# Kernel optimization log

Hardware: AMD Instinct MI355X
Metric: run time of the kernel (lower is better)

Reference implementation:

```python
import jax, jax.numpy as jnp
import numpy as np
from jax import lax

# db4 decomposition low-pass filter (pywt convention, ascending index)
DEC_LO = np.array([-0.010597401784997278, 0.032883011666982945, 0.030841381835986965,
                   -0.18703481171888114, -0.02798376941698385, 0.6308807679295904,
                   0.7148465705525415, 0.23037781330885523], dtype=np.float32)
L = 8
REC_LO = DEC_LO[::-1].copy()
DEC_HI = (REC_LO * ((-1.0) ** (np.arange(L) + 1))).astype(np.float32)
REC_HI = DEC_HI[::-1].copy()


def _dwt_last(x, lo, hi):
    """Single-level DWT along last axis, pywt 'symmetric' mode.
    Returns (cA, cD), each (..., (N+L-1)//2)."""
    ext = jnp.pad(x, [(0, 0)] * (x.ndim - 1) + [(L - 1, L - 1)], mode='symmetric')[..., 1:]
    z = ext.reshape(-1, 1, ext.shape[-1])
    # correlation with flipped filter == true convolution
    k = jnp.stack([lo[::-1], hi[::-1]])[:, None, :]  # (2,1,L)
    y = lax.conv_general_dilated(z, k, (2,), 'VALID', dimension_numbers=('NCH', 'OIH', 'NCH'))
    y = y.reshape(x.shape[:-1] + (2, y.shape[-1]))
    return y[..., 0, :], y[..., 1, :]


def _idwt_last(cA, cD, lo, hi):
    """Single-level inverse DWT along last axis (pywt upsampling convolution)."""
    n = cA.shape[-1]
    up = jnp.zeros(cA.shape[:-1] + (2, 2 * n - 1), cA.dtype)
    up = up.at[..., 0, ::2].set(cA).at[..., 1, ::2].set(cD)
    z = up.reshape(-1, 2, 2 * n - 1)
    k = jnp.stack([lo[::-1], hi[::-1]])[None, :, :]  # (1,2,L) -> sum of lo/hi branches
    y = lax.conv_general_dilated(z, k, (1,), [(L - 1, L - 1)], dimension_numbers=('NCH', 'OIH', 'NCH'))
    y = y[:, 0, L - 2: 2 * n]  # length 2n - L + 2
    return y.reshape(cA.shape[:-1] + (2 * n - L + 2,))


def dwt2d(x):
    lo, hi = jnp.asarray(DEC_LO), jnp.asarray(DEC_HI)
    a, d = _dwt_last(x, lo, hi)                       # along W
    aa, da = _dwt_last(a.swapaxes(-1, -2), lo, hi)    # along H
    ad, dd = _dwt_last(d.swapaxes(-1, -2), lo, hi)
    LL = aa.swapaxes(-1, -2)
    LH = da.swapaxes(-1, -2)   # cH: detail along H, approx along W
    HL = ad.swapaxes(-1, -2)   # cV: approx along H, detail along W
    HH = dd.swapaxes(-1, -2)
    return LL, LH, HL, HH


def idwt2d(LL, LH, HL, HH):
    lo, hi = jnp.asarray(REC_LO), jnp.asarray(REC_HI)
    a = _idwt_last(LL.swapaxes(-1, -2), LH.swapaxes(-1, -2), lo, hi).swapaxes(-1, -2)  # along H
    d = _idwt_last(HL.swapaxes(-1, -2), HH.swapaxes(-1, -2), lo, hi).swapaxes(-1, -2)
    return _idwt_last(a, d, lo, hi)  # along W


def attention_weight(x, c1w, c1b, c2w, gamma, beta, rmean, rvar):
    """x: (b, w, c, h). Max/mean pool over dim 1, 1x1 conv 2->1, depthwise conv1d
    over c channels, BatchNorm1d (eval), sigmoid gate."""
    feat = jnp.stack([x.max(axis=1), x.mean(axis=1)], axis=1)  # (b,2,c,h)
    y = jnp.einsum('i,bich->bch', c1w.reshape(2), feat) + c1b[0]  # (b,c,h)
    C = y.shape[1]
    p = (c2w.shape[-1] - 1) // 2
    y = lax.conv_general_dilated(y, c2w, (1,), [(p, p)], feature_group_count=C,
                                 dimension_numbers=('NCH', 'OIH', 'NCH'))
    y = (y - rmean[:, None]) * lax.rsqrt(rvar[:, None] + 1e-5) * gamma[:, None] + beta[:, None]
    return x * jax.nn.sigmoid(y)[:, None]


def _forward(x, lh_c1w, lh_c1b, lh_c2w, lh_g, lh_b, lh_m, lh_v,
             hl_c1w, hl_c1b, hl_c2w, hl_g, hl_b, hl_m, hl_v):
    LL, LH, HL, HH = dwt2d(x)
    LHp = attention_weight(LH.transpose(0, 3, 1, 2), lh_c1w, lh_c1b, lh_c2w, lh_g, lh_b, lh_m, lh_v).transpose(0, 2, 3, 1)
    HLp = attention_weight(HL.transpose(0, 2, 1, 3), hl_c1w, hl_c1b, hl_c2w, hl_g, hl_b, hl_m, hl_v).transpose(0, 2, 1, 3)
    rec = idwt2d(LL, LHp, HLp, HH)
    H, W = x.shape[-2], x.shape[-1]
    return x + rec[..., :H, :W]


def setup_inputs() -> dict:
    key = jax.random.key(0)
    ks = jax.random.split(key, 16)
    B, C, H, W, K = 8, 64, 512, 512, 3
    d = {"x": jax.random.normal(ks[0], (B, C, H, W), dtype=jnp.float32)}
    for i, pre in enumerate(["lh", "hl"]):
        base = 1 + 7 * i
        d[pre + "_c1w"] = jax.random.normal(ks[base + 0], (1, 2, 1, 1), dtype=jnp.float32) * 0.5
        d[pre + "_c1b"] = jax.random.normal(ks[base + 1], (1,), dtype=jnp.float32) * 0.1
        d[pre + "_c2w"] = jax.random.normal(ks[base + 2], (C, 1, K), dtype=jnp.float32) * 0.3
        d[pre + "_g"] = jnp.ones((C,), dtype=jnp.float32)
        d[pre + "_b"] = jnp.zeros((C,), dtype=jnp.float32)
        d[pre + "_m"] = jax.random.normal(ks[base + 3], (C,), dtype=jnp.float32) * 0.1
        d[pre + "_v"] = jax.random.uniform(ks[base + 4], (C,), dtype=jnp.float32, minval=0.5, maxval=1.5)
    return d


def reference(x, lh_c1w, lh_c1b, lh_c2w, lh_g, lh_b, lh_m, lh_v,
              hl_c1w, hl_c1b, hl_c2w, hl_g, hl_b, hl_m, hl_v):
    return _forward(x, lh_c1w, lh_c1b, lh_c2w, lh_g, lh_b, lh_m, lh_v,
                    hl_c1w, hl_c1b, hl_c2w, hl_g, hl_b, hl_m, hl_v)
```

## Files before the change

### kernel.cpp

```cpp
#include <hip/hip_runtime.h>

typedef _Float16 h16;
typedef _Float16 h16x2 __attribute__((ext_vector_type(2)));
typedef _Float16 h16x4 __attribute__((ext_vector_type(4)));
typedef _Float16 h16x8 __attribute__((ext_vector_type(8)));
typedef float f32x4 __attribute__((ext_vector_type(4)));

#if __has_builtin(__builtin_amdgcn_fdot2)
#define FDOT2(a, b, c) __builtin_amdgcn_fdot2((a), (b), (c), false)
#else
static __device__ __forceinline__ float FDOT2(h16x2 a, h16x2 b, float c) {
  return c + (float)a[0] * (float)b[0] + (float)a[1] * (float)b[1];
}
#endif

#define N_IMG 512
#define C_CH  64
#define H_IN  512
#define W_IN  512
#define NC    259
#define PITP  528
#define S2    ((size_t)NC * PITP)
#define GPIT  264
#define FSTRIP 17
#define LROWS  38

constexpr float DLO[8] = {
  -0.010597401784997278f,  0.032883011666982945f,  0.030841381835986965f, -0.18703481171888114f,
  -0.02798376941698385f,   0.6308807679295904f,    0.7148465705525415f,    0.23037781330885523f};
constexpr float DHI[8] = {
  -0.23037781330885523f,   0.7148465705525415f,   -0.6308807679295904f,   -0.02798376941698385f,
   0.18703481171888114f,   0.030841381835986965f, -0.032883011666982945f, -0.010597401784997278f};
constexpr float RLO[8] = {
   0.23037781330885523f,   0.7148465705525415f,    0.6308807679295904f,   -0.02798376941698385f,
  -0.18703481171888114f,   0.030841381835986965f,  0.032883011666982945f, -0.010597401784997278f};
constexpr float RHI[8] = {
  -0.010597401784997278f, -0.032883011666982945f,  0.030841381835986965f,  0.18703481171888114f,
  -0.02798376941698385f,  -0.6308807679295904f,    0.7148465705525415f,   -0.23037781330885523f};

__global__ __launch_bounds__(512) void k_fwd(const float* __restrict__ x,
                                             h16* __restrict__ wsh,
                                             float* __restrict__ stat) {
  __shared__ h16 sad[LROWS * PITP];
  const int p = blockIdx.x;
  const int w = (p & 7) * 1088 + (p >> 3);
  const int bc = w / FSTRIP;
  const int bx = w - bc * FSTRIP;
  const int h0 = bx * 16;
  const int hcount = min(16, NC - h0);
  const int nrows = 2 * hcount + 6;
  const int tid = threadIdx.x;
  const int wave = tid >> 6, lane = tid & 63;
  const float* xim = x + (size_t)bc * (H_IN * (size_t)W_IN);

  for (int j = wave; j < nrows; j += 8) {
    int r = 2 * h0 - 6 + j;
    r = r < 0 ? -r - 1 : (r >= H_IN ? 2 * H_IN - 1 - r : r);
    const float* xrow = xim + (size_t)r * W_IN;
    h16* sj = sad + j * PITP;
    const int base = lane ? 8 * lane - 8 : 0;
    const float4 q0 = *(const float4*)(xrow + base);
    const float4 q1 = *(const float4*)(xrow + base + 4);
    const float4 q2 = *(const float4*)(xrow + base + 8);
    const float4 q3 = *(const float4*)(xrow + base + 12);
    const float v[16] = {q0.x, q0.y, q0.z, q0.w, q1.x, q1.y, q1.z, q1.w,
                         q2.x, q2.y, q2.z, q2.w, q3.x, q3.y, q3.z, q3.w};
    if (lane == 0) {
      h16x8 o;
#pragma unroll
      for (int i = 0; i < 4; ++i) {
        float a = 0.f, d = 0.f;
#pragma unroll
        for (int m = 0; m < 8; ++m) {
          int pp = 2 * i + 1 - m; pp = pp < 0 ? -pp - 1 : pp;
          const float t = v[pp];
          a += DLO[m] * t; d += DHI[m] * t;
        }
        o[2 * i] = (h16)a; o[2 * i + 1] = (h16)d;
      }
      *(h16x8*)(sj) = o;
    } else {
      h16x8 o;
#pragma unroll
      for (int k = 0; k < 4; ++k) {
        float a = 0.f, d = 0.f;
#pragma unroll
        for (int m = 0; m < 8; ++m) {
          const float t = v[2 * k + 9 - m];
          a += DLO[m] * t; d += DHI[m] * t;
        }
        o[2 * k] = (h16)a; o[2 * k + 1] = (h16)d;
      }
      *(h16x8*)(sj + 8 * lane) = o;
      if (lane == 63) {
#pragma unroll
        for (int i = 256; i < 259; ++i) {
          float a = 0.f, d = 0.f;
#pragma unroll
          for (int m = 0; m < 8; ++m) {
            int pp = 2 * i + 1 - m; pp = pp >= 512 ? 1023 - pp : pp;
            const float t = v[pp - 496];
            a += DLO[m] * t; d += DHI[m] * t;
          }
          h16x2 o2; o2[0] = (h16)a; o2[1] = (h16)d;
          *(h16x2*)(sj + 2 * i) = o2;
        }
      }
    }
  }
  __syncthreads();

  const size_t obase = (size_t)bc * S2;
  const int ntask = hcount * 66;
  float rlh[3][4], rhl[3][4];
#pragma unroll
  for (int slot = 0; slot < 3; ++slot) {
    const int task = tid + slot * 512;
    if (task < ntask) {
      const int dh = task / 66, pq = task - dh * 66;
      h16x2 a0 = {0, 0}, a1 = {0, 0}, a2_ = {0, 0}, a3 = {0, 0};
#pragma unroll
      for (int m = 0; m < 8; ++m) {
        const int j = 2 * dh + 7 - m;
        const h16x8 pr = *(const h16x8*)(sad + j * PITP + 8 * pq);
        const h16x2 cf = {(h16)DHI[m], (h16)DLO[m]};
        const h16x2 p0 = {pr[0], pr[1]}, p1 = {pr[2], pr[3]};
        const h16x2 p2 = {pr[4], pr[5]}, p3 = {pr[6], pr[7]};
        a0 += cf * p0; a1 += cf * p1; a2_ += cf * p2; a3 += cf * p3;
      }
      if (pq == 64) { a3 = (h16x2){0, 0}; }
      if (pq == 65) { a0 = a1 = a2_ = a3 = (h16x2){0, 0}; }
      h16x8 o = {a0[0], a0[1], a1[0], a1[1], a2_[0], a2_[1], a3[0], a3[1]};
      *(h16x8*)(wsh + obase + (size_t)(h0 + dh) * PITP + 8 * pq) = o;
      rlh[slot][0] = (float)a0[0]; rlh[slot][1] = (float)a1[0];
      rlh[slot][2] = (float)a2_[0]; rlh[slot][3] = (float)a3[0];
      rhl[slot][0] = (float)a0[1]; rhl[slot][1] = (float)a1[1];
      rhl[slot][2] = (float)a2_[1]; rhl[slot][3] = (float)a3[1];
    }
  }
  __syncthreads();

  float* scol = (float*)sad;
  float* prmx = scol + 16 * 264;
  float* prsm = prmx + 1056;
#pragma unroll
  for (int slot = 0; slot < 3; ++slot) {
    const int task = tid + slot * 512;
    if (task < ntask) {
      const int dh = task / 66, pq = task - dh * 66;
      if (pq < 66) {
        *(float4*)(scol + dh * 264 + 4 * pq) =
            {rhl[slot][0], rhl[slot][1], rhl[slot][2], rhl[slot][3]};
      }
      if (pq == 65) {
        prmx[task] = -3.4e38f; prsm[task] = 0.f;
      } else {
        const float m01 = fmaxf(rlh[slot][0], rlh[slot][1]);
        const float m23 = (pq == 64) ? rlh[slot][2] : fmaxf(rlh[slot][2], rlh[slot][3]);
        prmx[task] = fmaxf(m01, m23);
        prsm[task] = rlh[slot][0] + rlh[slot][1] + rlh[slot][2] + rlh[slot][3];
      }
    }
  }
  __syncthreads();
  float* rsM = stat;
  float* rsS = stat + (size_t)N_IMG * 264;
  float* cpM = rsS + (size_t)N_IMG * 264;
  float* cpS = cpM + (size_t)N_IMG * FSTRIP * 264;
  for (int hh = wave; hh < hcount; hh += 8) {
    float m = prmx[hh * 66 + lane], s = prsm[hh * 66 + lane];
    if (lane == 0) {
      m = fmaxf(m, fmaxf(prmx[hh * 66 + 64], prmx[hh * 66 + 65]));
      s += prsm[hh * 66 + 64] + prsm[hh * 66 + 65];
    }
#pragma unroll
    for (int off = 32; off; off >>= 1) {
      m = fmaxf(m, __shfl_xor(m, off)); s += __shfl_xor(s, off);
    }
    if (lane == 0) {
      rsM[bc * 264 + h0 + hh] = m;
      rsS[bc * 264 + h0 + hh] = s;
    }
  }
  if (tid < 264) {
    float m = -3.4e38f, s = 0.f;
    for (int dh = 0; dh < hcount; ++dh) {
      const float vv = scol[dh * 264 + tid]; m = fmaxf(m, vv); s += vv;
    }
    const size_t cb = ((size_t)bc * FSTRIP + bx) * 264 + tid;
    cpM[cb] = m; cpS[cb] = s;
  }
}

__global__ __launch_bounds__(256) void k_gate(
    const float* __restrict__ stat, float* __restrict__ gout,
    const float* lc1w, const float* lc1b, const float* lc2w,
    const float* lg, const float* lb, const float* lm, const float* lv,
    const float* hc1w, const float* hc1b, const float* hc2w,
    const float* hg, const float* hb, const float* hm, const float* hv) {
  __shared__ float cmx[264], csm[264], y0a[264], y0b[264];
  const int bc = blockIdx.x;
  const int tid = threadIdx.x;
  const float* rsM = stat;
  const float* rsS = stat + (size_t)N_IMG * 264;
  const float* cpM = rsS + (size_t)N_IMG * 264;
  const float* cpS = cpM + (size_t)N_IMG * FSTRIP * 264;

  for (int col = tid; col < 264; col += 256) {
    float m = -3.4e38f, s = 0.f;
    for (int st = 0; st < FSTRIP; ++st) {
      const size_t cb = ((size_t)bc * FSTRIP + st) * 264 + col;
      m = fmaxf(m, cpM[cb]); s += cpS[cb];
    }
    cmx[col] = m; csm[col] = s;
  }
  __syncthreads();
  const float lw0 = lc1w[0], lw1 = lc1w[1], lbb0 = lc1b[0];
  const float hw0 = hc1w[0], hw1 = hc1w[1], hbb0 = hc1b[0];
  for (int idx = tid; idx < NC; idx += 256) {
    y0a[idx] = lw0 * rsM[bc * 264 + idx] + lw1 * (rsS[bc * 264 + idx] * (1.f / NC)) + lbb0;
    y0b[idx] = hw0 * cmx[idx] + hw1 * (csm[idx] * (1.f / NC)) + hbb0;
  }
  __syncthreads();
  const int c = bc & (C_CH - 1);
  const float lk0 = lc2w[c * 3], lk1 = lc2w[c * 3 + 1], lk2 = lc2w[c * 3 + 2];
  const float hk0 = hc2w[c * 3], hk1 = hc2w[c * 3 + 1], hk2 = hc2w[c * 3 + 2];
  const float lsc = rsqrtf(lv[c] + 1e-5f) * lg[c], lmu = lm[c], lbe = lb[c];
  const float hsc = rsqrtf(hv[c] + 1e-5f) * hg[c], hmu = hm[c], hbe = hb[c];
  for (int idx = tid; idx < NC; idx += 256) {
    float a = idx > 0 ? y0a[idx - 1] : 0.f;
    float b = y0a[idx];
    float d = idx < NC - 1 ? y0a[idx + 1] : 0.f;
    float y = lk0 * a + lk1 * b + lk2 * d;
    y = (y - lmu) * lsc + lbe;
    gout[(size_t)bc * GPIT + idx] = 1.f / (1.f + expf(-y)) - 1.f;

    a = idx > 0 ? y0b[idx - 1] : 0.f;
    b = y0b[idx];
    d = idx < NC - 1 ? y0b[idx + 1] : 0.f;
    y = hk0 * a + hk1 * b + hk2 * d;
    y = (y - hmu) * hsc + hbe;
    gout[(size_t)N_IMG * GPIT + (size_t)bc * GPIT + idx] = 1.f / (1.f + expf(-y)) - 1.f;
  }
}

__global__ __launch_bounds__(512) void k_inv(const h16* __restrict__ wsh,
                                             const float* __restrict__ gbuf,
                                             const float* __restrict__ x,
                                             float* __restrict__ out) {
  __shared__ h16 sBC[11 * PITP];
  __shared__ h16 ad2[16 * PITP];
  __shared__ h16 sghl16[264];
  const int p = blockIdx.x;
  const int w = (p & 7) * 2048 + (p >> 3);
  const int bc = w >> 5;
  const int t0 = (w & 31) * 16;
  const int u0 = t0 >> 1;
  const int tid = threadIdx.x;
  const h16* sub = wsh + (size_t)bc * S2;
  const float* glh = gbuf + (size_t)bc * GPIT;
  const float* ghl = gbuf + (size_t)N_IMG * GPIT + (size_t)bc * GPIT;

  if (tid < 264) sghl16[tid] = (h16)ghl[tid];

  for (int t = tid; t < 11 * 66; t += 512) {
    const int j = t / 66, pq = t - j * 66;
    const int u = u0 + j;
    const h16 glH = (h16)glh[u];
    const h16x2 cf = {glH, (h16)1.0f};
    const h16x8 pr = *(const h16x8*)(sub + (size_t)u * PITP + 8 * pq);
    h16x2 r0 = cf * (h16x2){pr[0], pr[1]};
    h16x2 r1 = cf * (h16x2){pr[2], pr[3]};
    h16x2 r2 = cf * (h16x2){pr[4], pr[5]};
    h16x2 r3 = cf * (h16x2){pr[6], pr[7]};
    h16x8 o = {r0[0], r0[1], r1[0], r1[1], r2[0], r2[1], r3[0], r3[1]};
    *(h16x8*)(sBC + j * PITP + 8 * pq) = o;
  }
  __syncthreads();

  for (int task = tid; task < 16 * 132; task += 512) {
    const int dt = task / 132, pq = task - dt * 132;
    const int par = dt & 1, lj0 = dt >> 1;
    h16x2 acc0 = {0, 0}, acc1 = {0, 0};
#pragma unroll
    for (int jj = 0; jj < 4; ++jj) {
      const int lj = lj0 + 3 - jj;
      const h16x2 cf = {(h16)(par ? RHI[1 + 2 * jj] : RHI[2 * jj]),
                        (h16)(par ? RLO[1 + 2 * jj] : RLO[2 * jj])};
      const h16x4 pr = *(const h16x4*)(sBC + lj * PITP + 4 * pq);
      acc0 += cf * (h16x2){pr[0], pr[1]};
      acc1 += cf * (h16x2){pr[2], pr[3]};
    }
    const h16x2 g2 = *(const h16x2*)(sghl16 + 2 * pq);
    const h16x2 cg0 = {(h16)1.0f, g2[0]};
    const h16x2 cg1 = {(h16)1.0f, g2[1]};
    acc0 *= cg0; acc1 *= cg1;
    h16x4 o = {acc0[0], acc0[1], acc1[0], acc1[1]};
    *(h16x4*)(ad2 + dt * PITP + 4 * pq) = o;
  }
  __syncthreads();

  for (int task = tid; task < 16 * 128; task += 512) {
    const int dt = task >> 7, r = task & 127;
    const h16* row = ad2 + dt * PITP + 4 * r;
    const h16x4 w0 = *(const h16x4*)(row);
    const h16x4 w1 = *(const h16x4*)(row + 4);
    const h16x2 w2 = *(const h16x2*)(row + 8);
    const h16x2 P[5] = {{w0[0], w0[1]}, {w0[2], w0[3]},
                        {w1[0], w1[1]}, {w1[2], w1[3]}, w2};
    float vv[4];
#pragma unroll
    for (int k = 0; k < 4; ++k) {
      const int base = k >> 1, par = k & 1;
      float s = 0.f;
#pragma unroll
      for (int jj = 0; jj < 4; ++jj) {
        const h16x2 cf = {(h16)RLO[par + 2 * jj], (h16)RHI[par + 2 * jj]};
        s = FDOT2(P[base + 3 - jj], cf, s);
      }
      vv[k] = s;
    }
    const size_t orow = ((size_t)bc * H_IN + (size_t)(t0 + dt)) * W_IN + 4 * r;
    const f32x4 xv = __builtin_nontemporal_load((const f32x4*)(x + orow));
    f32x4 ov;
    ov.x = 2.f * xv.x + vv[0]; ov.y = 2.f * xv.y + vv[1];
    ov.z = 2.f * xv.z + vv[2]; ov.w = 2.f * xv.w + vv[3];
    __builtin_nontemporal_store(ov, (f32x4*)(out + orow));
  }
}

extern "C" void kernel_launch(void* const* d_in, const int* in_sizes, int n_in,
                              void* d_out, int out_size, void* d_ws, size_t ws_size,
                              hipStream_t stream) {
  const float* x = (const float*)d_in[0];
  h16* wsh = (h16*)d_ws;
  float* statf = (float*)(wsh + (size_t)N_IMG * S2);
  float* gbuf = statf + 2 * (size_t)N_IMG * 264 + 2 * (size_t)N_IMG * FSTRIP * 264;
  float* out = (float*)d_out;

  k_fwd<<<dim3(FSTRIP * N_IMG), 512, 0, stream>>>(x, wsh, statf);
  k_gate<<<dim3(N_IMG), 256, 0, stream>>>(
      statf, gbuf,
      (const float*)d_in[1], (const float*)d_in[2], (const float*)d_in[3],
      (const float*)d_in[4], (const float*)d_in[5], (const float*)d_in[6], (const float*)d_in[7],
      (const float*)d_in[8], (const float*)d_in[9], (const float*)d_in[10],
      (const float*)d_in[11], (const float*)d_in[12], (const float*)d_in[13], (const float*)d_in[14]);
  k_inv<<<dim3(32 * N_IMG), 512, 0, stream>>>(wsh, gbuf, x, out);
}
```

Baseline: 370.3 us.

## Stream forward DWT over half-images with a ring buffer; enlarge inverse tiles

```diff
diff --git a/kernel.cpp b/kernel.cpp
--- a/kernel.cpp
+++ b/kernel.cpp
@@ -22,8 +22,7 @@
 #define PITP  528
 #define S2    ((size_t)NC * PITP)
 #define GPIT  264
-#define FSTRIP 17
-#define LROWS  38
+#define RING  38
 
 constexpr float DLO[8] = {
   -0.010597401784997278f,  0.032883011666982945f,  0.030841381835986965f, -0.18703481171888114f,
@@ -41,153 +40,171 @@
 __global__ __launch_bounds__(512) void k_fwd(const float* __restrict__ x,
                                              h16* __restrict__ wsh,
                                              float* __restrict__ stat) {
-  __shared__ h16 sad[LROWS * PITP];
+  __shared__ h16 sad[RING * PITP];
   const int p = blockIdx.x;
-  const int w = (p & 7) * 1088 + (p >> 3);
-  const int bc = w / FSTRIP;
-  const int bx = w - bc * FSTRIP;
-  const int h0 = bx * 16;
-  const int hcount = min(16, NC - h0);
-  const int nrows = 2 * hcount + 6;
+  const int w = (p & 7) * 128 + (p >> 3);
+  const int bc = w >> 1;
+  const int half = w & 1;
+  const int h_begin = half ? 130 : 0;
+  const int h_end = half ? 259 : 130;
   const int tid = threadIdx.x;
   const int wave = tid >> 6, lane = tid & 63;
   const float* xim = x + (size_t)bc * (H_IN * (size_t)W_IN);
-
-  for (int j = wave; j < nrows; j += 8) {
-    int r = 2 * h0 - 6 + j;
-    r = r < 0 ? -r - 1 : (r >= H_IN ? 2 * H_IN - 1 - r : r);
-    const float* xrow = xim + (size_t)r * W_IN;
-    h16* sj = sad + j * PITP;
-    const int base = lane ? 8 * lane - 8 : 0;
-    const float4 q0 = *(const float4*)(xrow + base);
-    const float4 q1 = *(const float4*)(xrow + base + 4);
-    const float4 q2 = *(const float4*)(xrow + base + 8);
-    const float4 q3 = *(const float4*)(xrow + base + 12);
-    const float v[16] = {q0.x, q0.y, q0.z, q0.w, q1.x, q1.y, q1.z, q1.w,
-                         q2.x, q2.y, q2.z, q2.w, q3.x, q3.y, q3.z, q3.w};
-    if (lane == 0) {
-      h16x8 o;
-#pragma unroll
-      for (int i = 0; i < 4; ++i) {
-        float a = 0.f, d = 0.f;
-#pragma unroll
-        for (int m = 0; m < 8; ++m) {
-          int pp = 2 * i + 1 - m; pp = pp < 0 ? -pp - 1 : pp;
-          const float t = v[pp];
-          a += DLO[m] * t; d += DHI[m] * t;
-        }
-        o[2 * i] = (h16)a; o[2 * i + 1] = (h16)d;
-      }
-      *(h16x8*)(sj) = o;
-    } else {
-      h16x8 o;
-#pragma unroll
-      for (int k = 0; k < 4; ++k) {
-        float a = 0.f, d = 0.f;
-#pragma unroll
-        for (int m = 0; m < 8; ++m) {
-          const float t = v[2 * k + 9 - m];
-          a += DLO[m] * t; d += DHI[m] * t;
-        }
-        o[2 * k] = (h16)a; o[2 * k + 1] = (h16)d;
-      }
-      *(h16x8*)(sj + 8 * lane) = o;
-      if (lane == 63) {
-#pragma unroll
-        for (int i = 256; i < 259; ++i) {
-          float a = 0.f, d = 0.f;
-#pragma unroll
-          for (int m = 0; m < 8; ++m) {
-            int pp = 2 * i + 1 - m; pp = pp >= 512 ? 1023 - pp : pp;
-            const float t = v[pp - 496];
-            a += DLO[m] * t; d += DHI[m] * t;
-          }
-          h16x2 o2; o2[0] = (h16)a; o2[1] = (h16)d;
-          *(h16x2*)(sj + 2 * i) = o2;
-        }
-      }
-    }
-  }
-  __syncthreads();
-
   const size_t obase = (size_t)bc * S2;
-  const int ntask = hcount * 66;
-  float rlh[3][4], rhl[3][4];
-#pragma unroll
-  for (int slot = 0; slot < 3; ++slot) {
-    const int task = tid + slot * 512;
-    if (task < ntask) {
-      const int dh = task / 66, pq = task - dh * 66;
-      h16x2 a0 = {0, 0}, a1 = {0, 0}, a2_ = {0, 0}, a3 = {0, 0};
-#pragma unroll
-      for (int m = 0; m < 8; ++m) {
-        const int j = 2 * dh + 7 - m;
-        const h16x8 pr = *(const h16x8*)(sad + j * PITP + 8 * pq);
-        const h16x2 cf = {(h16)DHI[m], (h16)DLO[m]};
-        const h16x2 p0 = {pr[0], pr[1]}, p1 = {pr[2], pr[3]};
-        const h16x2 p2 = {pr[4], pr[5]}, p3 = {pr[6], pr[7]};
-        a0 += cf * p0; a1 += cf * p1; a2_ += cf * p2; a3 += cf * p3;
-      }
-      if (pq == 64) { a3 = (h16x2){0, 0}; }
-      if (pq == 65) { a0 = a1 = a2_ = a3 = (h16x2){0, 0}; }
-      h16x8 o = {a0[0], a0[1], a1[0], a1[1], a2_[0], a2_[1], a3[0], a3[1]};
-      *(h16x8*)(wsh + obase + (size_t)(h0 + dh) * PITP + 8 * pq) = o;
-      rlh[slot][0] = (float)a0[0]; rlh[slot][1] = (float)a1[0];
-      rlh[slot][2] = (float)a2_[0]; rlh[slot][3] = (float)a3[0];
-      rhl[slot][0] = (float)a0[1]; rhl[slot][1] = (float)a1[1];
-      rhl[slot][2] = (float)a2_[1]; rhl[slot][3] = (float)a3[1];
-    }
-  }
-  __syncthreads();
-
-  float* scol = (float*)sad;
-  float* prmx = scol + 16 * 264;
-  float* prsm = prmx + 1056;
-#pragma unroll
-  for (int slot = 0; slot < 3; ++slot) {
-    const int task = tid + slot * 512;
-    if (task < ntask) {
-      const int dh = task / 66, pq = task - dh * 66;
-      if (pq < 66) {
-        *(float4*)(scol + dh * 264 + 4 * pq) =
-            {rhl[slot][0], rhl[slot][1], rhl[slot][2], rhl[slot][3]};
-      }
-      if (pq == 65) {
-        prmx[task] = -3.4e38f; prsm[task] = 0.f;
-      } else {
-        const float m01 = fmaxf(rlh[slot][0], rlh[slot][1]);
-        const float m23 = (pq == 64) ? rlh[slot][2] : fmaxf(rlh[slot][2], rlh[slot][3]);
-        prmx[task] = fmaxf(m01, m23);
-        prsm[task] = rlh[slot][0] + rlh[slot][1] + rlh[slot][2] + rlh[slot][3];
-      }
-    }
-  }
-  __syncthreads();
+
   float* rsM = stat;
   float* rsS = stat + (size_t)N_IMG * 264;
   float* cpM = rsS + (size_t)N_IMG * 264;
-  float* cpS = cpM + (size_t)N_IMG * FSTRIP * 264;
-  for (int hh = wave; hh < hcount; hh += 8) {
-    float m = prmx[hh * 66 + lane], s = prsm[hh * 66 + lane];
-    if (lane == 0) {
-      m = fmaxf(m, fmaxf(prmx[hh * 66 + 64], prmx[hh * 66 + 65]));
-      s += prsm[hh * 66 + 64] + prsm[hh * 66 + 65];
-    }
-#pragma unroll
-    for (int off = 32; off; off >>= 1) {
-      m = fmaxf(m, __shfl_xor(m, off)); s += __shfl_xor(s, off);
-    }
-    if (lane == 0) {
-      rsM[bc * 264 + h0 + hh] = m;
-      rsS[bc * 264 + h0 + hh] = s;
-    }
-  }
+  float* cpS = cpM + (size_t)N_IMG * 2 * 264;
+
+  float c0m[4], c0s[4], c1m[4], c1s[4];
+#pragma unroll
+  for (int k = 0; k < 4; ++k) {
+    c0m[k] = -3.4e38f; c0s[k] = 0.f; c1m[k] = -3.4e38f; c1s[k] = 0.f;
+  }
+
+  int rx_next = 2 * h_begin - 6;
+  for (int h0 = h_begin; h0 < h_end; h0 += 16) {
+    const int hcount = min(16, h_end - h0);
+    const int rx_hi = 2 * (h0 + hcount - 1) + 1;
+
+    for (int j = rx_next + wave; j <= rx_hi; j += 8) {
+      int r = j;
+      r = r < 0 ? -r - 1 : (r >= H_IN ? 2 * H_IN - 1 - r : r);
+      const float* xrow = xim + (size_t)r * W_IN;
+      h16* sj = sad + ((j + RING) % RING) * PITP;
+      const int base = lane ? 8 * lane - 8 : 0;
+      const float4 q0 = *(const float4*)(xrow + base);
+      const float4 q1 = *(const float4*)(xrow + base + 4);
+      const float4 q2 = *(const float4*)(xrow + base + 8);
+      const float4 q3 = *(const float4*)(xrow + base + 12);
+      const float v[16] = {q0.x, q0.y, q0.z, q0.w, q1.x, q1.y, q1.z, q1.w,
+                           q2.x, q2.y, q2.z, q2.w, q3.x, q3.y, q3.z, q3.w};
+      if (lane == 0) {
+        h16x8 o;
+#pragma unroll
+        for (int i = 0; i < 4; ++i) {
+          float a = 0.f, d = 0.f;
+#pragma unroll
+          for (int m = 0; m < 8; ++m) {
+            int pp = 2 * i + 1 - m; pp = pp < 0 ? -pp - 1 : pp;
+            const float t = v[pp];
+            a += DLO[m] * t; d += DHI[m] * t;
+          }
+          o[2 * i] = (h16)a; o[2 * i + 1] = (h16)d;
+        }
+        *(h16x8*)(sj) = o;
+      } else {
+        h16x8 o;
+#pragma unroll
+        for (int k = 0; k < 4; ++k) {
+          float a = 0.f, d = 0.f;
+#pragma unroll
+          for (int m = 0; m < 8; ++m) {
+            const float t = v[2 * k + 9 - m];
+            a += DLO[m] * t; d += DHI[m] * t;
+          }
+          o[2 * k] = (h16)a; o[2 * k + 1] = (h16)d;
+        }
+        *(h16x8*)(sj + 8 * lane) = o;
+        if (lane == 63) {
+#pragma unroll
+          for (int i = 256; i < 259; ++i) {
+            float a = 0.f, d = 0.f;
+#pragma unroll
+            for (int m = 0; m < 8; ++m) {
+              int pp = 2 * i + 1 - m; pp = pp >= 512 ? 1023 - pp : pp;
+              const float t = v[pp - 496];
+              a += DLO[m] * t; d += DHI[m] * t;
+            }
+            h16x2 o2; o2[0] = (h16)a; o2[1] = (h16)d;
+            *(h16x2*)(sj + 2 * i) = o2;
+          }
+        }
+      }
+    }
+    rx_next = rx_hi + 1;
+    __syncthreads();
+
+    for (int dh = wave; dh < hcount; dh += 8) {
+      const int h = h0 + dh;
+      const int s0 = (2 * h + 1) % RING;
+      float rowm = -3.4e38f, rowsum = 0.f;
+#pragma unroll
+      for (int pass = 0; pass < 2; ++pass) {
+        const int pq = lane + 64 * pass;
+        if (pq < 66) {
+          h16x2 a0 = {0, 0}, a1 = {0, 0}, a2_ = {0, 0}, a3 = {0, 0};
+#pragma unroll
+          for (int m = 0; m < 8; ++m) {
+            int slot = s0 - m; slot = slot < 0 ? slot + RING : slot;
+            const h16x8 pr = *(const h16x8*)(sad + slot * PITP + 8 * pq);
+            const h16x2 cf = {(h16)DHI[m], (h16)DLO[m]};
+            a0 += cf * (h16x2){pr[0], pr[1]};
+            a1 += cf * (h16x2){pr[2], pr[3]};
+            a2_ += cf * (h16x2){pr[4], pr[5]};
+            a3 += cf * (h16x2){pr[6], pr[7]};
+          }
+          if (pq == 64) { a3 = (h16x2){0, 0}; }
+          if (pq == 65) { a0 = a1 = a2_ = a3 = (h16x2){0, 0}; }
+          h16x8 o = {a0[0], a0[1], a1[0], a1[1], a2_[0], a2_[1], a3[0], a3[1]};
+          *(h16x8*)(wsh + obase + (size_t)h * PITP + 8 * pq) = o;
+          const float l0 = (float)a0[0], l1 = (float)a1[0];
+          const float l2 = (float)a2_[0], l3 = (float)a3[0];
+          const float g0 = (float)a0[1], g1 = (float)a1[1];
+          const float g2 = (float)a2_[1], g3 = (float)a3[1];
+          if (pq < 65) {
+            const float m01 = fmaxf(l0, l1);
+            const float m23 = (pq == 64) ? l2 : fmaxf(l2, l3);
+            rowm = fmaxf(rowm, fmaxf(m01, m23));
+            rowsum += l0 + l1 + l2 + l3;
+          }
+          if (pass == 0) {
+            c0m[0] = fmaxf(c0m[0], g0); c0s[0] += g0;
+            c0m[1] = fmaxf(c0m[1], g1); c0s[1] += g1;
+            c0m[2] = fmaxf(c0m[2], g2); c0s[2] += g2;
+            c0m[3] = fmaxf(c0m[3], g3); c0s[3] += g3;
+          } else {
+            c1m[0] = fmaxf(c1m[0], g0); c1s[0] += g0;
+            c1m[1] = fmaxf(c1m[1], g1); c1s[1] += g1;
+            c1m[2] = fmaxf(c1m[2], g2); c1s[2] += g2;
+            c1m[3] = fmaxf(c1m[3], g3); c1s[3] += g3;
+          }
+        }
+      }
+#pragma unroll
+      for (int off = 32; off; off >>= 1) {
+        rowm = fmaxf(rowm, __shfl_xor(rowm, off));
+        rowsum += __shfl_xor(rowsum, off);
+      }
+      if (lane == 0) {
+        rsM[bc * 264 + h] = rowm;
+        rsS[bc * 264 + h] = rowsum;
+      }
+    }
+    __syncthreads();
+  }
+
+  float* wbuf = (float*)sad;
+  float* wm = wbuf + wave * 528;
+  float* wsv = wm + 264;
+#pragma unroll
+  for (int k = 0; k < 4; ++k) { wm[4 * lane + k] = c0m[k]; wsv[4 * lane + k] = c0s[k]; }
+  if (lane < 2) {
+#pragma unroll
+    for (int k = 0; k < 4; ++k) {
+      wm[256 + 4 * lane + k] = c1m[k]; wsv[256 + 4 * lane + k] = c1s[k];
+    }
+  }
+  __syncthreads();
   if (tid < 264) {
     float m = -3.4e38f, s = 0.f;
-    for (int dh = 0; dh < hcount; ++dh) {
-      const float vv = scol[dh * 264 + tid]; m = fmaxf(m, vv); s += vv;
-    }
-    const size_t cb = ((size_t)bc * FSTRIP + bx) * 264 + tid;
+#pragma unroll
+    for (int w8 = 0; w8 < 8; ++w8) {
+      m = fmaxf(m, wbuf[w8 * 528 + tid]);
+      s += wbuf[w8 * 528 + 264 + tid];
+    }
+    const size_t cb = ((size_t)bc * 2 + half) * 264 + tid;
     cpM[cb] = m; cpS[cb] = s;
   }
 }
@@ -204,15 +221,13 @@
   const float* rsM = stat;
   const float* rsS = stat + (size_t)N_IMG * 264;
   const float* cpM = rsS + (size_t)N_IMG * 264;
-  const float* cpS = cpM + (size_t)N_IMG * FSTRIP * 264;
+  const float* cpS = cpM + (size_t)N_IMG * 2 * 264;
 
   for (int col = tid; col < 264; col += 256) {
-    float m = -3.4e38f, s = 0.f;
-    for (int st = 0; st < FSTRIP; ++st) {
-      const size_t cb = ((size_t)bc * FSTRIP + st) * 264 + col;
-      m = fmaxf(m, cpM[cb]); s += cpS[cb];
-    }
-    cmx[col] = m; csm[col] = s;
+    const size_t cb0 = ((size_t)bc * 2) * 264 + col;
+    const size_t cb1 = ((size_t)bc * 2 + 1) * 264 + col;
+    cmx[col] = fmaxf(cpM[cb0], cpM[cb1]);
+    csm[col] = cpS[cb0] + cpS[cb1];
   }
   __syncthreads();
   const float lw0 = lc1w[0], lw1 = lc1w[1], lbb0 = lc1b[0];
@@ -248,13 +263,13 @@
                                              const float* __restrict__ gbuf,
                                              const float* __restrict__ x,
                                              float* __restrict__ out) {
-  __shared__ h16 sBC[11 * PITP];
+  __shared__ h16 sBC[19 * PITP];
   __shared__ h16 ad2[16 * PITP];
   __shared__ h16 sghl16[264];
   const int p = blockIdx.x;
-  const int w = (p & 7) * 2048 + (p >> 3);
-  const int bc = w >> 5;
-  const int t0 = (w & 31) * 16;
+  const int w = (p & 7) * 1024 + (p >> 3);
+  const int bc = w >> 4;
+  const int t0 = (w & 15) * 32;
   const int u0 = t0 >> 1;
   const int tid = threadIdx.x;
   const h16* sub = wsh + (size_t)bc * S2;
@@ -263,7 +278,7 @@
 
   if (tid < 264) sghl16[tid] = (h16)ghl[tid];
 
-  for (int t = tid; t < 11 * 66; t += 512) {
+  for (int t = tid; t < 19 * 66; t += 512) {
     const int j = t / 66, pq = t - j * 66;
     const int u = u0 + j;
     const h16 glH = (h16)glh[u];
@@ -278,54 +293,60 @@
   }
   __syncthreads();
 
-  for (int task = tid; task < 16 * 132; task += 512) {
-    const int dt = task / 132, pq = task - dt * 132;
-    const int par = dt & 1, lj0 = dt >> 1;
-    h16x2 acc0 = {0, 0}, acc1 = {0, 0};
-#pragma unroll
-    for (int jj = 0; jj < 4; ++jj) {
-      const int lj = lj0 + 3 - jj;
-      const h16x2 cf = {(h16)(par ? RHI[1 + 2 * jj] : RHI[2 * jj]),
-                        (h16)(par ? RLO[1 + 2 * jj] : RLO[2 * jj])};
-      const h16x4 pr = *(const h16x4*)(sBC + lj * PITP + 4 * pq);
-      acc0 += cf * (h16x2){pr[0], pr[1]};
-      acc1 += cf * (h16x2){pr[2], pr[3]};
-    }
-    const h16x2 g2 = *(const h16x2*)(sghl16 + 2 * pq);
-    const h16x2 cg0 = {(h16)1.0f, g2[0]};
-    const h16x2 cg1 = {(h16)1.0f, g2[1]};
-    acc0 *= cg0; acc1 *= cg1;
-    h16x4 o = {acc0[0], acc0[1], acc1[0], acc1[1]};
-    *(h16x4*)(ad2 + dt * PITP + 4 * pq) = o;
-  }
-  __syncthreads();
-
-  for (int task = tid; task < 16 * 128; task += 512) {
-    const int dt = task >> 7, r = task & 127;
-    const h16* row = ad2 + dt * PITP + 4 * r;
-    const h16x4 w0 = *(const h16x4*)(row);
-    const h16x4 w1 = *(const h16x4*)(row + 4);
-    const h16x2 w2 = *(const h16x2*)(row + 8);
-    const h16x2 P[5] = {{w0[0], w0[1]}, {w0[2], w0[3]},
-                        {w1[0], w1[1]}, {w1[2], w1[3]}, w2};
-    float vv[4];
-#pragma unroll
-    for (int k = 0; k < 4; ++k) {
-      const int base = k >> 1, par = k & 1;
-      float s = 0.f;
+#pragma unroll
+  for (int batch = 0; batch < 2; ++batch) {
+    for (int task = tid; task < 16 * 132; task += 512) {
+      const int dtl = task / 132, pq = task - dtl * 132;
+      const int dt = batch * 16 + dtl;
+      const int par = dt & 1, lj0 = dt >> 1;
+      h16x2 acc0 = {0, 0}, acc1 = {0, 0};
 #pragma unroll
       for (int jj = 0; jj < 4; ++jj) {
-        const h16x2 cf = {(h16)RLO[par + 2 * jj], (h16)RHI[par + 2 * jj]};
-        s = FDOT2(P[base + 3 - jj], cf, s);
-      }
-      vv[k] = s;
-    }
-    const size_t orow = ((size_t)bc * H_IN + (size_t)(t0 + dt)) * W_IN + 4 * r;
-    const f32x4 xv = __builtin_nontemporal_load((const f32x4*)(x + orow));
-    f32x4 ov;
-    ov.x = 2.f * xv.x + vv[0]; ov.y = 2.f * xv.y + vv[1];
-    ov.z = 2.f * xv.z + vv[2]; ov.w = 2.f * xv.w + vv[3];
-    __builtin_nontemporal_store(ov, (f32x4*)(out + orow));
+        const int lj = lj0 + 3 - jj;
+        const h16x2 cf = {(h16)(par ? RHI[1 + 2 * jj] : RHI[2 * jj]),
+                          (h16)(par ? RLO[1 + 2 * jj] : RLO[2 * jj])};
+        const h16x4 pr = *(const h16x4*)(sBC + lj * PITP + 4 * pq);
+        acc0 += cf * (h16x2){pr[0], pr[1]};
+        acc1 += cf * (h16x2){pr[2], pr[3]};
+      }
+      const h16x2 g2 = *(const h16x2*)(sghl16 + 2 * pq);
+      const h16x2 cg0 = {(h16)1.0f, g2[0]};
+      const h16x2 cg1 = {(h16)1.0f, g2[1]};
+      acc0 *= cg0; acc1 *= cg1;
+      h16x4 o = {acc0[0], acc0[1], acc1[0], acc1[1]};
+      *(h16x4*)(ad2 + dtl * PITP + 4 * pq) = o;
+    }
+    __syncthreads();
+
+    for (int task = tid; task < 16 * 128; task += 512) {
+      const int dtl = task >> 7, r = task & 127;
+      const h16* row = ad2 + dtl * PITP + 4 * r;
+      const h16x4 w0 = *(const h16x4*)(row);
+      const h16x4 w1 = *(const h16x4*)(row + 4);
+      const h16x2 w2 = *(const h16x2*)(row + 8);
+      const h16x2 P[5] = {{w0[0], w0[1]}, {w0[2], w0[3]},
+                          {w1[0], w1[1]}, {w1[2], w1[3]}, w2};
+      float vv[4];
+#pragma unroll
+      for (int k = 0; k < 4; ++k) {
+        const int base = k >> 1, par = k & 1;
+        float s = 0.f;
+#pragma unroll
+        for (int jj = 0; jj < 4; ++jj) {
+          const h16x2 cf = {(h16)RLO[par + 2 * jj], (h16)RHI[par + 2 * jj]};
+          s = FDOT2(P[base + 3 - jj], cf, s);
+        }
+        vv[k] = s;
+      }
+      const size_t orow =
+          ((size_t)bc * H_IN + (size_t)(t0 + batch * 16 + dtl)) * W_IN + 4 * r;
+      const f32x4 xv = __builtin_nontemporal_load((const f32x4*)(x + orow));
+      f32x4 ov;
+      ov.x = 2.f * xv.x + vv[0]; ov.y = 2.f * xv.y + vv[1];
+      ov.z = 2.f * xv.z + vv[2]; ov.w = 2.f * xv.w + vv[3];
+      __builtin_nontemporal_store(ov, (f32x4*)(out + orow));
+    }
+    if (batch == 0) __syncthreads();
   }
 }
 
@@ -335,15 +356,15 @@
   const float* x = (const float*)d_in[0];
   h16* wsh = (h16*)d_ws;
   float* statf = (float*)(wsh + (size_t)N_IMG * S2);
-  float* gbuf = statf + 2 * (size_t)N_IMG * 264 + 2 * (size_t)N_IMG * FSTRIP * 264;
+  float* gbuf = statf + 2 * (size_t)N_IMG * 264 + 2 * (size_t)N_IMG * 2 * 264;
   float* out = (float*)d_out;
 
-  k_fwd<<<dim3(FSTRIP * N_IMG), 512, 0, stream>>>(x, wsh, statf);
+  k_fwd<<<dim3(1024), 512, 0, stream>>>(x, wsh, statf);
   k_gate<<<dim3(N_IMG), 256, 0, stream>>>(
       statf, gbuf,
       (const float*)d_in[1], (const float*)d_in[2], (const float*)d_in[3],
       (const float*)d_in[4], (const float*)d_in[5], (const float*)d_in[6], (const float*)d_in[7],
       (const float*)d_in[8], (const float*)d_in[9], (const float*)d_in[10],
       (const float*)d_in[11], (const float*)d_in[12], (const float*)d_in[13], (const float*)d_in[14]);
-  k_inv<<<dim3(32 * N_IMG), 512, 0, stream>>>(wsh, gbuf, x, out);
-}
+  k_inv<<<dim3(16 * N_IMG), 512, 0, stream>>>(wsh, gbuf, x, out);
+}
```

New measurement: 429.3 us. 1.16x slower.
